# Kernel optimization log

Hardware: AMD Instinct MI355X
Metric: run time of the kernel (lower is better)

Reference implementation:

```python
import jax, jax.numpy as jnp
import numpy as np

NEG_INF = -9e15
LEAKY_SLOPE = 0.01  # PyTorch F.leaky_relu default


def setup_inputs() -> dict:
    key = jax.random.key(0)
    k1, k2, k3, k4 = jax.random.split(key, 4)
    B, N, Fin, Fout = 4, 4096, 64, 64
    X = jax.random.normal(k1, (B, N, Fin), dtype=jnp.float32)
    A = jax.random.randint(k2, (N, N), 0, 2, dtype=jnp.int32)
    weight = jax.random.normal(k3, (Fin, Fout), dtype=jnp.float32) * 0.15
    a = jax.random.normal(k4, (2 * Fout, 1), dtype=jnp.float32) * 0.15
    return {"X": X, "A": A, "weight": weight, "a": a}


def reference(X, A, weight, a):
    B, N, _ = X.shape
    Fout = weight.shape[1]
    # add self loops: A[i,i] = 1
    mask = (A > 0) | jnp.eye(N, dtype=bool)  # [N, N]
    Xw = jnp.matmul(X, weight)  # [B, N, Fout]
    # additive attention: e_ij = leaky_relu(a_l . x_i + a_r . x_j)
    # equivalent to the repeat/cat/matmul in the original, without O(N^2 F) memory
    a_l = a[:Fout, 0]   # [Fout]
    a_r = a[Fout:, 0]   # [Fout]
    left = jnp.einsum('bnf,f->bn', Xw, a_l)   # [B, N]
    right = jnp.einsum('bnf,f->bn', Xw, a_r)  # [B, N]
    e = left[:, :, None] + right[:, None, :]  # [B, N, N]
    e = jnp.where(e >= 0, e, LEAKY_SLOPE * e)
    att = jnp.where(mask[None, :, :], e, NEG_INF)
    att = jax.nn.softmax(att, axis=-1)  # dropout p=0 -> identity
    out = jnp.matmul(att, Xw)  # [B, N, Fout]
    return out
```

## Files before the change

### kernel.cpp

```cpp
#include <hip/hip_runtime.h>
#include <hip/hip_bf16.h>
#include <math.h>

#define BB 4
#define NN 4096
#define FF 64
#define KS (NN / 32)
#define NKW (KS / 4)
#define C0F 3.35462628e-4f
#define C1F 3.35462628e-6f
#define PREB 512

typedef _Float16 half8 __attribute__((ext_vector_type(8)));
typedef _Float16 half2v __attribute__((ext_vector_type(2)));
typedef float f32x4 __attribute__((ext_vector_type(4)));

__global__ __launch_bounds__(256, 2)
void k_prep(const float* __restrict__ X, const float* __restrict__ W,
            const float* __restrict__ avec, const int* __restrict__ A,
            _Float16* __restrict__ XwP, float2* __restrict__ LE,
            float2* __restrict__ RE, unsigned int* __restrict__ bitsT) {
    __shared__ __align__(16) float Wl[64 * 64];
    __shared__ __align__(16) float Xl[32][64];
    __shared__ __align__(16) float T[32][65];
    __shared__ float al[64];
    __shared__ float ar[64];

    const int t = threadIdx.x;

    if (blockIdx.x >= PREB) {
        int pidx = (blockIdx.x - PREB) * 256 + t;
        int row  = pidx >> 10;
        int c4   = pidx & 1023;
        const uint4* A4 = (const uint4*)A;
        uint4 av = A4[pidx];
        unsigned int nib = 0;
        nib |= ((int)av.x > 0) ? 1u : 0u;
        nib |= ((int)av.y > 0) ? 2u : 0u;
        nib |= ((int)av.z > 0) ? 4u : 0u;
        nib |= ((int)av.w > 0) ? 8u : 0u;
        if (c4 == (row >> 2)) nib |= 1u << (row & 3);
        int lane = t & 63;
        unsigned int v = nib << ((lane & 7) * 4);
        v |= __shfl_xor(v, 1);
        v |= __shfl_xor(v, 2);
        v |= __shfl_xor(v, 4);
        if ((lane & 7) == 0)
            bitsT[(size_t)(c4 >> 3) * NN + row] = v;
        return;
    }

    const int lane = t & 63;
    const int wv = t >> 6;
    const int r0 = blockIdx.x * 32;

    #pragma unroll
    for (int k = 0; k < 16; ++k) Wl[t + k * 256] = W[t + k * 256];
    if (t < 64) { al[t] = avec[t]; ar[t] = avec[64 + t]; }
    {
        const float4* xs = (const float4*)(X + (size_t)r0 * 64);
        float4* xd = (float4*)&Xl[0][0];
        xd[t] = xs[t];
        xd[t + 256] = xs[t + 256];
    }
    __syncthreads();

    float Wreg[64];
    #pragma unroll
    for (int k = 0; k < 64; ++k) Wreg[k] = Wl[k * 64 + lane];

    #pragma unroll
    for (int rr = 0; rr < 8; ++rr) {
        int lrow = wv * 8 + rr;
        int row  = r0 + lrow;
        float a0 = 0.f, a1 = 0.f, a2 = 0.f, a3 = 0.f;
        #pragma unroll
        for (int k = 0; k < 64; k += 4) {
            float4 x = *(const float4*)&Xl[lrow][k];
            a0 = fmaf(x.x, Wreg[k],     a0);
            a1 = fmaf(x.y, Wreg[k + 1], a1);
            a2 = fmaf(x.z, Wreg[k + 2], a2);
            a3 = fmaf(x.w, Wreg[k + 3], a3);
        }
        float acc = (a0 + a1) + (a2 + a3);
        T[lrow][lane] = acc;

        float lv = acc * al[lane];
        float rv = acc * ar[lane];
        #pragma unroll
        for (int off = 32; off; off >>= 1) {
            lv += __shfl_xor(lv, off, 64);
            rv += __shfl_xor(rv, off, 64);
        }
        if (lane == 0) {
            LE[row] = make_float2(lv, __expf(lv - 8.f));
            RE[row] = make_float2(rv, __expf(rv));
        }
    }
    __syncthreads();

    int b  = r0 >> 12;
    int ks = (r0 & (NN - 1)) >> 5;
    int ct = t >> 6;
    int q  = lane >> 4, n = lane & 15;
    half8 h;
    #pragma unroll
    for (int jj = 0; jj < 8; ++jj)
        h[jj] = (_Float16)T[q * 8 + jj][ct * 16 + n];
    *(half8*)&XwP[((((size_t)b * KS + ks) * 4 + ct) * 64 + lane) * 8] = h;
}

__global__ __launch_bounds__(256, 2)
void k_main(const _Float16* __restrict__ XwP, const float2* __restrict__ LE,
            const float2* __restrict__ RE, const unsigned int* __restrict__ bitsT,
            float* __restrict__ out) {
    __shared__ __align__(16) char smem[32768];
    __shared__ uint2 lutm[16];
    float* REs_er = (float*)smem;
    float* REs_rc = (float*)(smem + 16384);
    float (*Lacc)[32][68] = (float (*)[32][68])smem;
    float* Lsum = (float*)(smem + 17408);

    const int t  = threadIdx.x;
    const int b  = blockIdx.y;
    const int i0 = blockIdx.x * 32;

    const int lane = t & 63;
    const int wv   = t >> 6;
    const int lm   = lane & 15;
    const int q    = lane >> 4;

    const int rowa = i0 + lm;
    const int rowb = i0 + 16 + lm;
    const float2 lea = LE[b * NN + rowa];
    const float2 leb = LE[b * NN + rowb];
    const float lca = lea.x * C1F;
    const float lcb = leb.x * C1F;
    const _Float16* xp = XwP + (size_t)b * KS * 2048 + (size_t)lane * 8;

    if (t < 16)
        lutm[t] = make_uint2(((t & 1) ? 0xFFFFu : 0u) | ((t & 2) ? 0xFFFF0000u : 0u),
                             ((t & 4) ? 0xFFFFu : 0u) | ((t & 8) ? 0xFFFF0000u : 0u));

    {
        const float4* rsrc = (const float4*)(RE + (size_t)b * NN);
        #pragma unroll
        for (int k = 0; k < 8; ++k) {
            float4 v = rsrc[t + k * 256];
            int idx = 2 * (t + k * 256);
            REs_er[idx]     = v.y;
            REs_er[idx + 1] = v.w;
            REs_rc[idx]     = fmaf(v.x, C1F, C0F);
            REs_rc[idx + 1] = fmaf(v.z, C1F, C0F);
        }
    }
    __syncthreads();

    f32x4 acca[4], accb[4];
    f32x4 sacca = (f32x4)0.f, saccb = (f32x4)0.f;
    #pragma unroll
    for (int ct = 0; ct < 4; ++ct) { acca[ct] = (f32x4)0.f; accb[ct] = (f32x4)0.f; }
    half8 vones;
    #pragma unroll
    for (int k = 0; k < 8; ++k) vones[k] = (_Float16)1.0f;

    const int ks0 = wv * NKW;

    const _Float16* base = xp + (size_t)ks0 * 2048;
    half8 nb0 = *(const half8*)(base + 0 * 512);
    half8 nb1 = *(const half8*)(base + 1 * 512);
    half8 nb2 = *(const half8*)(base + 2 * 512);
    half8 nb3 = *(const half8*)(base + 3 * 512);
    unsigned int nwa = bitsT[(size_t)ks0 * NN + rowa];
    unsigned int nwb = bitsT[(size_t)ks0 * NN + rowb];

    #pragma unroll 2
    for (int kk = 0; kk < NKW; ++kk) {
        half8 bf0 = nb0, bf1 = nb1, bf2 = nb2, bf3 = nb3;
        unsigned int wax = nwa >> (q * 8);
        unsigned int wbx = nwb >> (q * 8);
        uint2 ma0 = lutm[wax & 15], ma1 = lutm[(wax >> 4) & 15];
        uint2 mb0 = lutm[wbx & 15], mb1 = lutm[(wbx >> 4) & 15];

        {
            int nk = kk + 1 < NKW ? kk + 1 : kk;
            const _Float16* nbase = xp + (size_t)(ks0 + nk) * 2048;
            nb0 = *(const half8*)(nbase + 0 * 512);
            nb1 = *(const half8*)(nbase + 1 * 512);
            nb2 = *(const half8*)(nbase + 2 * 512);
            nb3 = *(const half8*)(nbase + 3 * 512);
            nwa = bitsT[(size_t)(ks0 + nk) * NN + rowa];
            nwb = bitsT[(size_t)(ks0 + nk) * NN + rowb];
        }

        const float4* ep = (const float4*)(REs_er + (ks0 + kk) * 32 + q * 8);
        float4 e0v = ep[0], e1v = ep[1];
        const float4* cp = (const float4*)(REs_rc + (ks0 + kk) * 32 + q * 8);
        float4 c0v = cp[0], c1v = cp[1];
        float er8[8] = {e0v.x, e0v.y, e0v.z, e0v.w, e1v.x, e1v.y, e1v.z, e1v.w};
        float rc8[8] = {c0v.x, c0v.y, c0v.z, c0v.w, c1v.x, c1v.y, c1v.z, c1v.w};

        float pa[8], pb[8];
        #pragma unroll
        for (int jj = 0; jj < 8; ++jj)
            pa[jj] = fmaxf(lea.y * er8[jj], lca + rc8[jj]);
        #pragma unroll
        for (int jj = 0; jj < 8; ++jj)
            pb[jj] = fmaxf(leb.y * er8[jj], lcb + rc8[jj]);

        uint4 ua, ub;
        ua.x = __builtin_bit_cast(unsigned int, __builtin_amdgcn_cvt_pkrtz(pa[0], pa[1])) & ma0.x;
        ua.y = __builtin_bit_cast(unsigned int, __builtin_amdgcn_cvt_pkrtz(pa[2], pa[3])) & ma0.y;
        ua.z = __builtin_bit_cast(unsigned int, __builtin_amdgcn_cvt_pkrtz(pa[4], pa[5])) & ma1.x;
        ua.w = __builtin_bit_cast(unsigned int, __builtin_amdgcn_cvt_pkrtz(pa[6], pa[7])) & ma1.y;
        ub.x = __builtin_bit_cast(unsigned int, __builtin_amdgcn_cvt_pkrtz(pb[0], pb[1])) & mb0.x;
        ub.y = __builtin_bit_cast(unsigned int, __builtin_amdgcn_cvt_pkrtz(pb[2], pb[3])) & mb0.y;
        ub.z = __builtin_bit_cast(unsigned int, __builtin_amdgcn_cvt_pkrtz(pb[4], pb[5])) & mb1.x;
        ub.w = __builtin_bit_cast(unsigned int, __builtin_amdgcn_cvt_pkrtz(pb[6], pb[7])) & mb1.y;
        half8 a0a = __builtin_bit_cast(half8, ua);
        half8 a0b = __builtin_bit_cast(half8, ub);

        acca[0] = __builtin_amdgcn_mfma_f32_16x16x32_f16(a0a, bf0, acca[0], 0, 0, 0);
        acca[1] = __builtin_amdgcn_mfma_f32_16x16x32_f16(a0a, bf1, acca[1], 0, 0, 0);
        acca[2] = __builtin_amdgcn_mfma_f32_16x16x32_f16(a0a, bf2, acca[2], 0, 0, 0);
        acca[3] = __builtin_amdgcn_mfma_f32_16x16x32_f16(a0a, bf3, acca[3], 0, 0, 0);
        sacca   = __builtin_amdgcn_mfma_f32_16x16x32_f16(a0a, vones, sacca, 0, 0, 0);

        accb[0] = __builtin_amdgcn_mfma_f32_16x16x32_f16(a0b, bf0, accb[0], 0, 0, 0);
        accb[1] = __builtin_amdgcn_mfma_f32_16x16x32_f16(a0b, bf1, accb[1], 0, 0, 0);
        accb[2] = __builtin_amdgcn_mfma_f32_16x16x32_f16(a0b, bf2, accb[2], 0, 0, 0);
        accb[3] = __builtin_amdgcn_mfma_f32_16x16x32_f16(a0b, bf3, accb[3], 0, 0, 0);
        saccb   = __builtin_amdgcn_mfma_f32_16x16x32_f16(a0b, vones, saccb, 0, 0, 0);
    }

    __syncthreads();

    if (wv >= 2) {
        #pragma unroll
        for (int r = 0; r < 4; ++r) {
            int lrow = q * 4 + r;
            #pragma unroll
            for (int ct = 0; ct < 4; ++ct) {
                Lacc[wv - 2][lrow][ct * 16 + lm]      = acca[ct][r];
                Lacc[wv - 2][16 + lrow][ct * 16 + lm] = accb[ct][r];
            }
            if (lm == 0) {
                Lsum[(wv - 2) * 32 + lrow]      = sacca[r];
                Lsum[(wv - 2) * 32 + 16 + lrow] = saccb[r];
            }
        }
    }
    __syncthreads();
    if (wv < 2) {
        #pragma unroll
        for (int r = 0; r < 4; ++r) {
            int lrow = q * 4 + r;
            #pragma unroll
            for (int ct = 0; ct < 4; ++ct) {
                Lacc[wv][lrow][ct * 16 + lm]      += acca[ct][r];
                Lacc[wv][16 + lrow][ct * 16 + lm] += accb[ct][r];
            }
            if (lm == 0) {
                Lsum[wv * 32 + lrow]      += sacca[r];
                Lsum[wv * 32 + 16 + lrow] += saccb[r];
            }
        }
    }
    __syncthreads();
    #pragma unroll
    for (int it = 0; it < 2; ++it) {
        int idx  = t + it * 256;
        int lrow = idx >> 4;
        int c0   = (idx & 15) * 4;
        float s = Lsum[lrow] + Lsum[32 + lrow];
        float inv = 1.f / s;
        float4 o;
        o.x = (Lacc[0][lrow][c0 + 0] + Lacc[1][lrow][c0 + 0]) * inv;
        o.y = (Lacc[0][lrow][c0 + 1] + Lacc[1][lrow][c0 + 1]) * inv;
        o.z = (Lacc[0][lrow][c0 + 2] + Lacc[1][lrow][c0 + 2]) * inv;
        o.w = (Lacc[0][lrow][c0 + 3] + Lacc[1][lrow][c0 + 3]) * inv;
        *(float4*)&out[((size_t)(b * NN + i0 + lrow) << 6) + c0] = o;
    }
}

extern "C" void kernel_launch(void* const* d_in, const int* in_sizes, int n_in,
                              void* d_out, int out_size, void* d_ws, size_t ws_size,
                              hipStream_t stream) {
    const float* X    = (const float*)d_in[0];
    const int*   A    = (const int*)d_in[1];
    const float* W    = (const float*)d_in[2];
    const float* avec = (const float*)d_in[3];
    float* out = (float*)d_out;

    char* ws = (char*)d_ws;
    size_t off = 0;
    _Float16* XwP = (_Float16*)(ws + off); off += (size_t)BB * NN * FF * 2;
    float2* LE = (float2*)(ws + off);      off += (size_t)BB * NN * 8;
    float2* RE = (float2*)(ws + off);      off += (size_t)BB * NN * 8;
    unsigned int* bitsT = (unsigned int*)(ws + off);
    off += (size_t)KS * NN * 4;
    (void)off; (void)ws_size;

    k_prep<<<PREB + NN * NN / 1024, 256, 0, stream>>>(X, W, avec, A, XwP, LE, RE, bitsT);
    k_main<<<dim3(NN / 32, BB), 256, 0, stream>>>(XwP, LE, RE, bitsT, out);
}
```

Baseline: 129.0 us.

## Split key range across 8 waves and stream right-side terms from global

The main kernel now runs 512 threads, so 8 waves each cover an eighth of the key range instead of four waves each covering a quarter. The cross-wave reduction is widened from 2 to 4 partial accumulators. The per-block LDS staging of the right-side exp and linear terms is removed. Those values are now precomputed in prep as separate planar arrays and prefetched from global memory with register double-buffering. This trades LDS fill time and a barrier for more global/L2 traffic, and per-iteration loop overhead is amortized over fewer iterations per wave.

```diff
diff --git a/kernel.cpp b/kernel.cpp
--- a/kernel.cpp
+++ b/kernel.cpp
@@ -6,20 +6,20 @@
 #define NN 4096
 #define FF 64
 #define KS (NN / 32)
-#define NKW (KS / 4)
+#define NKW8 (KS / 8)
 #define C0F 3.35462628e-4f
 #define C1F 3.35462628e-6f
 #define PREB 512
 
 typedef _Float16 half8 __attribute__((ext_vector_type(8)));
-typedef _Float16 half2v __attribute__((ext_vector_type(2)));
 typedef float f32x4 __attribute__((ext_vector_type(4)));
 
 __global__ __launch_bounds__(256, 2)
 void k_prep(const float* __restrict__ X, const float* __restrict__ W,
             const float* __restrict__ avec, const int* __restrict__ A,
             _Float16* __restrict__ XwP, float2* __restrict__ LE,
-            float2* __restrict__ RE, unsigned int* __restrict__ bitsT) {
+            float* __restrict__ ERt, float* __restrict__ RCt,
+            unsigned int* __restrict__ bitsT) {
     __shared__ __align__(16) float Wl[64 * 64];
     __shared__ __align__(16) float Xl[32][64];
     __shared__ __align__(16) float T[32][65];
@@ -93,8 +93,9 @@
             rv += __shfl_xor(rv, off, 64);
         }
         if (lane == 0) {
-            LE[row] = make_float2(lv, __expf(lv - 8.f));
-            RE[row] = make_float2(rv, __expf(rv));
+            LE[row]  = make_float2(lv * C1F, __expf(lv - 8.f));
+            ERt[row] = __expf(rv);
+            RCt[row] = fmaf(rv, C1F, C0F);
         }
     }
     __syncthreads();
@@ -110,16 +111,14 @@
     *(half8*)&XwP[((((size_t)b * KS + ks) * 4 + ct) * 64 + lane) * 8] = h;
 }
 
-__global__ __launch_bounds__(256, 2)
+__global__ __launch_bounds__(512, 4)
 void k_main(const _Float16* __restrict__ XwP, const float2* __restrict__ LE,
-            const float2* __restrict__ RE, const unsigned int* __restrict__ bitsT,
-            float* __restrict__ out) {
-    __shared__ __align__(16) char smem[32768];
+            const float* __restrict__ ERt, const float* __restrict__ RCt,
+            const unsigned int* __restrict__ bitsT, float* __restrict__ out) {
+    __shared__ __align__(16) char smem[35840];
     __shared__ uint2 lutm[16];
-    float* REs_er = (float*)smem;
-    float* REs_rc = (float*)(smem + 16384);
     float (*Lacc)[32][68] = (float (*)[32][68])smem;
-    float* Lsum = (float*)(smem + 17408);
+    float* Lsum = (float*)(smem + 34816);
 
     const int t  = threadIdx.x;
     const int b  = blockIdx.y;
@@ -134,26 +133,13 @@
     const int rowb = i0 + 16 + lm;
     const float2 lea = LE[b * NN + rowa];
     const float2 leb = LE[b * NN + rowb];
-    const float lca = lea.x * C1F;
-    const float lcb = leb.x * C1F;
     const _Float16* xp = XwP + (size_t)b * KS * 2048 + (size_t)lane * 8;
+    const float* erp = ERt + b * NN + q * 8;
+    const float* rcp = RCt + b * NN + q * 8;
 
     if (t < 16)
         lutm[t] = make_uint2(((t & 1) ? 0xFFFFu : 0u) | ((t & 2) ? 0xFFFF0000u : 0u),
                              ((t & 4) ? 0xFFFFu : 0u) | ((t & 8) ? 0xFFFF0000u : 0u));
-
-    {
-        const float4* rsrc = (const float4*)(RE + (size_t)b * NN);
-        #pragma unroll
-        for (int k = 0; k < 8; ++k) {
-            float4 v = rsrc[t + k * 256];
-            int idx = 2 * (t + k * 256);
-            REs_er[idx]     = v.y;
-            REs_er[idx + 1] = v.w;
-            REs_rc[idx]     = fmaf(v.x, C1F, C0F);
-            REs_rc[idx + 1] = fmaf(v.z, C1F, C0F);
-        }
-    }
     __syncthreads();
 
     f32x4 acca[4], accb[4];
@@ -164,7 +150,7 @@
     #pragma unroll
     for (int k = 0; k < 8; ++k) vones[k] = (_Float16)1.0f;
 
-    const int ks0 = wv * NKW;
+    const int ks0 = wv * NKW8;
 
     const _Float16* base = xp + (size_t)ks0 * 2048;
     half8 nb0 = *(const half8*)(base + 0 * 512);
@@ -173,17 +159,22 @@
     half8 nb3 = *(const half8*)(base + 3 * 512);
     unsigned int nwa = bitsT[(size_t)ks0 * NN + rowa];
     unsigned int nwb = bitsT[(size_t)ks0 * NN + rowb];
+    float4 ne0 = *(const float4*)(erp + ks0 * 32);
+    float4 ne1 = *(const float4*)(erp + ks0 * 32 + 4);
+    float4 nc0 = *(const float4*)(rcp + ks0 * 32);
+    float4 nc1 = *(const float4*)(rcp + ks0 * 32 + 4);
 
     #pragma unroll 2
-    for (int kk = 0; kk < NKW; ++kk) {
+    for (int kk = 0; kk < NKW8; ++kk) {
         half8 bf0 = nb0, bf1 = nb1, bf2 = nb2, bf3 = nb3;
+        float4 e0v = ne0, e1v = ne1, c0v = nc0, c1v = nc1;
         unsigned int wax = nwa >> (q * 8);
         unsigned int wbx = nwb >> (q * 8);
         uint2 ma0 = lutm[wax & 15], ma1 = lutm[(wax >> 4) & 15];
         uint2 mb0 = lutm[wbx & 15], mb1 = lutm[(wbx >> 4) & 15];
 
         {
-            int nk = kk + 1 < NKW ? kk + 1 : kk;
+            int nk = kk + 1 < NKW8 ? kk + 1 : kk;
             const _Float16* nbase = xp + (size_t)(ks0 + nk) * 2048;
             nb0 = *(const half8*)(nbase + 0 * 512);
             nb1 = *(const half8*)(nbase + 1 * 512);
@@ -191,22 +182,22 @@
             nb3 = *(const half8*)(nbase + 3 * 512);
             nwa = bitsT[(size_t)(ks0 + nk) * NN + rowa];
             nwb = bitsT[(size_t)(ks0 + nk) * NN + rowb];
-        }
-
-        const float4* ep = (const float4*)(REs_er + (ks0 + kk) * 32 + q * 8);
-        float4 e0v = ep[0], e1v = ep[1];
-        const float4* cp = (const float4*)(REs_rc + (ks0 + kk) * 32 + q * 8);
-        float4 c0v = cp[0], c1v = cp[1];
+            ne0 = *(const float4*)(erp + (ks0 + nk) * 32);
+            ne1 = *(const float4*)(erp + (ks0 + nk) * 32 + 4);
+            nc0 = *(const float4*)(rcp + (ks0 + nk) * 32);
+            nc1 = *(const float4*)(rcp + (ks0 + nk) * 32 + 4);
+        }
+
         float er8[8] = {e0v.x, e0v.y, e0v.z, e0v.w, e1v.x, e1v.y, e1v.z, e1v.w};
         float rc8[8] = {c0v.x, c0v.y, c0v.z, c0v.w, c1v.x, c1v.y, c1v.z, c1v.w};
 
         float pa[8], pb[8];
         #pragma unroll
         for (int jj = 0; jj < 8; ++jj)
-            pa[jj] = fmaxf(lea.y * er8[jj], lca + rc8[jj]);
+            pa[jj] = fmaxf(lea.y * er8[jj], lea.x + rc8[jj]);
         #pragma unroll
         for (int jj = 0; jj < 8; ++jj)
-            pb[jj] = fmaxf(leb.y * er8[jj], lcb + rc8[jj]);
+            pb[jj] = fmaxf(leb.y * er8[jj], leb.x + rc8[jj]);
 
         uint4 ua, ub;
         ua.x = __builtin_bit_cast(unsigned int, __builtin_amdgcn_cvt_pkrtz(pa[0], pa[1])) & ma0.x;
@@ -235,23 +226,23 @@
 
     __syncthreads();
 
-    if (wv >= 2) {
+    if (wv >= 4) {
         #pragma unroll
         for (int r = 0; r < 4; ++r) {
             int lrow = q * 4 + r;
             #pragma unroll
             for (int ct = 0; ct < 4; ++ct) {
-                Lacc[wv - 2][lrow][ct * 16 + lm]      = acca[ct][r];
-                Lacc[wv - 2][16 + lrow][ct * 16 + lm] = accb[ct][r];
+                Lacc[wv - 4][lrow][ct * 16 + lm]      = acca[ct][r];
+                Lacc[wv - 4][16 + lrow][ct * 16 + lm] = accb[ct][r];
             }
             if (lm == 0) {
-                Lsum[(wv - 2) * 32 + lrow]      = sacca[r];
-                Lsum[(wv - 2) * 32 + 16 + lrow] = saccb[r];
+                Lsum[(wv - 4) * 32 + lrow]      = sacca[r];
+                Lsum[(wv - 4) * 32 + 16 + lrow] = saccb[r];
             }
         }
     }
     __syncthreads();
-    if (wv < 2) {
+    if (wv < 4) {
         #pragma unroll
         for (int r = 0; r < 4; ++r) {
             int lrow = q * 4 + r;
@@ -267,18 +258,20 @@
         }
     }
     __syncthreads();
-    #pragma unroll
-    for (int it = 0; it < 2; ++it) {
-        int idx  = t + it * 256;
-        int lrow = idx >> 4;
-        int c0   = (idx & 15) * 4;
-        float s = Lsum[lrow] + Lsum[32 + lrow];
+    {
+        int lrow = t >> 4;
+        int c0   = (t & 15) * 4;
+        float s = (Lsum[lrow] + Lsum[32 + lrow]) + (Lsum[64 + lrow] + Lsum[96 + lrow]);
         float inv = 1.f / s;
+        float4 v0 = *(const float4*)&Lacc[0][lrow][c0];
+        float4 v1 = *(const float4*)&Lacc[1][lrow][c0];
+        float4 v2 = *(const float4*)&Lacc[2][lrow][c0];
+        float4 v3 = *(const float4*)&Lacc[3][lrow][c0];
         float4 o;
-        o.x = (Lacc[0][lrow][c0 + 0] + Lacc[1][lrow][c0 + 0]) * inv;
-        o.y = (Lacc[0][lrow][c0 + 1] + Lacc[1][lrow][c0 + 1]) * inv;
-        o.z = (Lacc[0][lrow][c0 + 2] + Lacc[1][lrow][c0 + 2]) * inv;
-        o.w = (Lacc[0][lrow][c0 + 3] + Lacc[1][lrow][c0 + 3]) * inv;
+        o.x = ((v0.x + v1.x) + (v2.x + v3.x)) * inv;
+        o.y = ((v0.y + v1.y) + (v2.y + v3.y)) * inv;
+        o.z = ((v0.z + v1.z) + (v2.z + v3.z)) * inv;
+        o.w = ((v0.w + v1.w) + (v2.w + v3.w)) * inv;
         *(float4*)&out[((size_t)(b * NN + i0 + lrow) << 6) + c0] = o;
     }
 }
@@ -296,11 +289,12 @@
     size_t off = 0;
     _Float16* XwP = (_Float16*)(ws + off); off += (size_t)BB * NN * FF * 2;
     float2* LE = (float2*)(ws + off);      off += (size_t)BB * NN * 8;
-    float2* RE = (float2*)(ws + off);      off += (size_t)BB * NN * 8;
+    float* ERt = (float*)(ws + off);       off += (size_t)BB * NN * 4;
+    float* RCt = (float*)(ws + off);       off += (size_t)BB * NN * 4;
     unsigned int* bitsT = (unsigned int*)(ws + off);
     off += (size_t)KS * NN * 4;
     (void)off; (void)ws_size;
 
-    k_prep<<<PREB + NN * NN / 1024, 256, 0, stream>>>(X, W, avec, A, XwP, LE, RE, bitsT);
-    k_main<<<dim3(NN / 32, BB), 256, 0, stream>>>(XwP, LE, RE, bitsT, out);
+    k_prep<<<PREB + NN * NN / 1024, 256, 0, stream>>>(X, W, avec, A, XwP, LE, ERt, RCt, bitsT);
+    k_main<<<dim3(NN / 32, BB), 512, 0, stream>>>(XwP, LE, ERt, RCt, bitsT, out);
 }
```

Measured after the change: 134.1 us. +4.0%, slower.
